# Optimization experiments

Measured on AMD Instinct MI355X. Metric: run time of the kernel, lower is better.

## Reference

```python
import jax, jax.numpy as jnp
import numpy as np
from jax import lax
from jax.scipy.linalg import expm

B, T, H, NCLS = 256, 784, 512, 10


def setup_inputs() -> dict:
    key = jax.random.key(0)
    ks = jax.random.split(key, 6)
    inputs = jax.random.normal(ks[0], (B, T), dtype=jnp.float32)
    # faithful to Model: fixed permutation from RandomState(92916)
    permutation = jnp.asarray(np.random.RandomState(92916).permutation(T), dtype=jnp.int64)
    W_skew = jax.random.normal(ks[1], (H, H), dtype=jnp.float32) * 0.05  # free param for skew-symmetric A
    W_in = jax.random.normal(ks[2], (H, 1), dtype=jnp.float32)            # Linear(1, H, bias=False)
    b_mod = jax.random.uniform(ks[3], (H,), dtype=jnp.float32, minval=-0.01, maxval=0.01)  # modrelu bias
    W_lin = jax.random.normal(ks[4], (NCLS, H), dtype=jnp.float32) * 0.05
    b_lin = jax.random.normal(ks[5], (NCLS,), dtype=jnp.float32) * 0.05
    return {"inputs": inputs, "permutation": permutation, "W_skew": W_skew,
            "W_in": W_in, "b_mod": b_mod, "W_lin": W_lin, "b_lin": b_lin}


def reference(inputs, permutation, W_skew, W_in, b_mod, W_lin, b_lin):
    # permuted-pixel input sequence: [B, T]
    x = inputs[:, permutation]
    # expm parametrization of the orthogonal recurrent kernel:
    # A = triu(W,1) - triu(W,1)^T (skew-symmetric), Borth = expm(A) is orthogonal
    Au = jnp.triu(W_skew, 1)
    Borth = expm(Au - Au.T)  # [H, H]
    # precompute all input projections: Linear(1,H) on each scalar pixel -> [T, B, H]
    proj = x.T[:, :, None] * W_in[:, 0][None, None, :]

    def step(h, u):
        pre = u + h @ Borth                                  # [B, H]
        h_new = jnp.sign(pre) * jax.nn.relu(jnp.abs(pre) + b_mod)  # modrelu
        return h_new, None

    h0 = jnp.zeros((inputs.shape[0], W_in.shape[0]), dtype=inputs.dtype)
    hT, _ = lax.scan(step, h0, proj)
    return hT @ W_lin.T + b_lin  # [B, 10]
```

## Files before the change

kernel.cpp:

```cpp
#include <hip/hip_runtime.h>

#define TSTEPS 784
#define BATCH  256
#define HDIM   512
#define NCLS   10
#define NGRP   16
#define WGPG   8

typedef __bf16 bf16x8 __attribute__((ext_vector_type(8)));
typedef float  f32x4  __attribute__((ext_vector_type(4)));
typedef unsigned uint4v __attribute__((ext_vector_type(4)));
typedef unsigned long long u64;
typedef unsigned short u16;

static __device__ __forceinline__ u16 f2bf(float f) {
  unsigned u = __builtin_bit_cast(unsigned, f);
  u += 0x7fffu + ((u >> 16) & 1u);
  return (u16)(u >> 16);
}
static __device__ __forceinline__ float bf2f(unsigned s) {
  unsigned u = s << 16;
  return __builtin_bit_cast(float, u);
}

__global__ __launch_bounds__(256) void gather_xp(const float* __restrict__ in,
                                                 const int* __restrict__ perm,
                                                 float* __restrict__ xp) {
  int t = blockIdx.x;
  int b = threadIdx.x;
  int p = perm[t];
  p = (p < 0) ? 0 : (p >= TSTEPS ? TSTEPS - 1 : p);
  xp[t * BATCH + b] = in[b * TSTEPS + p];
}

__global__ __launch_bounds__(256) void build_X(const float* __restrict__ W,
                                               float* __restrict__ X) {
  int idx = blockIdx.x * 256 + threadIdx.x;
  int i = idx >> 9, j = idx & 511;
  float v = 0.f;
  if (j > i) v = W[i * HDIM + j];
  else if (i > j) v = -W[j * HDIM + i];
  X[idx] = v * 0.03125f;
}

__global__ __launch_bounds__(256) void axpyI(float* __restrict__ P,
                                             const float* __restrict__ X, float coef) {
  int idx = blockIdx.x * 256 + threadIdx.x;
  int i = idx >> 9, j = idx & 511;
  P[idx] = coef * X[idx] + ((i == j) ? 1.f : 0.f);
}

__global__ __launch_bounds__(256) void gemm512(float* __restrict__ C,
                                               const float* __restrict__ A,
                                               const float* __restrict__ B,
                                               float alpha, int addI) {
  __shared__ float As[16][68];
  __shared__ float Bs[16][68];
  const int tx = threadIdx.x, ty = threadIdx.y;
  const int tid = ty * 16 + tx;
  const int ib = blockIdx.y, jb = blockIdx.x;
  const int ra = tid >> 2, ca = (tid & 3) << 2;
  const int rb = tid >> 4, cb = (tid & 15) << 2;
  float acc[4][4] = {};
  for (int kt = 0; kt < HDIM / 16; ++kt) {
    f32x4 av = *(const f32x4*)(A + (ib * 64 + ra) * HDIM + kt * 16 + ca);
    f32x4 bv = *(const f32x4*)(B + (kt * 16 + rb) * HDIM + jb * 64 + cb);
    __syncthreads();
    As[ca + 0][ra] = av[0];
    As[ca + 1][ra] = av[1];
    As[ca + 2][ra] = av[2];
    As[ca + 3][ra] = av[3];
    *(f32x4*)&Bs[rb][cb] = bv;
    __syncthreads();
#pragma unroll
    for (int kk = 0; kk < 16; ++kk) {
      f32x4 a4 = *(const f32x4*)&As[kk][ty << 2];
      f32x4 b4 = *(const f32x4*)&Bs[kk][tx << 2];
#pragma unroll
      for (int u = 0; u < 4; ++u)
#pragma unroll
        for (int v = 0; v < 4; ++v) acc[u][v] = fmaf(a4[u], b4[v], acc[u][v]);
    }
  }
#pragma unroll
  for (int u = 0; u < 4; ++u)
#pragma unroll
    for (int v = 0; v < 4; ++v) {
      int r = ib * 64 + (ty << 2) + u, c = jb * 64 + (tx << 2) + v;
      float val = alpha * acc[u][v];
      if (addI && r == c) val += 1.f;
      C[r * HDIM + c] = val;
    }
}

__global__ __launch_bounds__(256, 1) void rnn_main(
    const float* __restrict__ xp, const float* __restrict__ Borth,
    const float* __restrict__ W_in, const float* __restrict__ b_mod,
    const float* __restrict__ W_lin, const float* __restrict__ b_lin,
    u16* __restrict__ h0hi, u16* __restrict__ h0lo, u16* __restrict__ h1hi,
    u16* __restrict__ h1lo, unsigned* __restrict__ flags, float* __restrict__ out) {
  __shared__ unsigned tileHi[4096], tileLo[4096];

  const int wg = blockIdx.x;
  const int gb = wg & 15;
  const int cg = wg >> 4;
  const int tid = threadIdx.x;
  const int wave = tid >> 6;
  const int lane = tid & 63;
  const int quad = lane >> 4;
  const int l16 = lane & 15;
  const int colg = (cg << 6) + (wave << 4) + l16;

  bf16x8 Bfh[16], Bfl[16];
#pragma unroll
  for (int ki = 0; ki < 16; ++ki) {
#pragma unroll
    for (int j = 0; j < 8; ++j) {
      int k = (ki << 5) + (quad << 3) + j;
      float v = Borth[k * HDIM + colg];
      u16 hb = f2bf(v);
      u16 lb = f2bf(v - bf2f(hb));
      Bfh[ki][j] = __builtin_bit_cast(__bf16, hb);
      Bfl[ki][j] = __builtin_bit_cast(__bf16, lb);
    }
  }
  const float win = W_in[colg];
  const float bm = b_mod[colg];

  u16* const g0h = h0hi + (gb << 13);
  u16* const g0l = h0lo + (gb << 13);
  u16* const g1h = h1hi + (gb << 13);
  u16* const g1l = h1lo + (gb << 13);
  unsigned* const myflag = flags + ((gb << 3) + cg) * 32;
  unsigned* const gflags = flags + (gb << 3) * 32;
  const unsigned swz = (unsigned)((l16 & 7) << 2);

  for (int t = 0; t < TSTEPS; ++t) {
    const u64* __restrict__ cH = (const u64*)((t & 1) ? g1h : g0h);
    const u64* __restrict__ cL = (const u64*)((t & 1) ? g1l : g0l);
    u16* __restrict__ nH = (t & 1) ? g0h : g1h;
    u16* __restrict__ nL = (t & 1) ? g0l : g1l;

    u64 qh[8], ql[8];
#pragma unroll
    for (int i = 0; i < 8; ++i) {
      qh[i] = __hip_atomic_load(cH + tid + (i << 8), __ATOMIC_RELAXED,
                                __HIP_MEMORY_SCOPE_AGENT);
      ql[i] = __hip_atomic_load(cL + tid + (i << 8), __ATOMIC_RELAXED,
                                __HIP_MEMORY_SCOPE_AGENT);
    }
#pragma unroll
    for (int i = 0; i < 8; ++i) {
      int f = tid + (i << 8);
      int r = f >> 7;
      unsigned du = (unsigned)(f & 127) << 1;
      unsigned phys = ((unsigned)r << 8) | (du ^ ((r & 7) << 2));
      *(u64*)(tileHi + phys) = qh[i];
      *(u64*)(tileLo + phys) = ql[i];
    }
    __syncthreads();

    f32x4 a_hh = {0.f, 0.f, 0.f, 0.f};
    f32x4 a_lh = {0.f, 0.f, 0.f, 0.f};
    f32x4 a_hl = {0.f, 0.f, 0.f, 0.f};
#pragma unroll
    for (int ki = 0; ki < 16; ++ki) {
      unsigned dcol0 = (unsigned)((ki << 4) + (quad << 2));
      unsigned off = ((unsigned)l16 << 8) + (dcol0 ^ swz);
      bf16x8 ah = __builtin_bit_cast(bf16x8, *(const uint4v*)(tileHi + off));
      bf16x8 al = __builtin_bit_cast(bf16x8, *(const uint4v*)(tileLo + off));
      a_hh = __builtin_amdgcn_mfma_f32_16x16x32_bf16(ah, Bfh[ki], a_hh, 0, 0, 0);
      a_lh = __builtin_amdgcn_mfma_f32_16x16x32_bf16(al, Bfh[ki], a_lh, 0, 0, 0);
      a_hl = __builtin_amdgcn_mfma_f32_16x16x32_bf16(ah, Bfl[ki], a_hl, 0, 0, 0);
    }

    const f32x4 xps = *(const f32x4*)(xp + t * BATCH + (gb << 4) + (quad << 2));
#pragma unroll
    for (int r = 0; r < 4; ++r) {
      float pre = a_hh[r] + a_lh[r] + a_hl[r] + xps[r] * win;
      float mm = fmaxf(fabsf(pre) + bm, 0.f);
      float hv = (pre > 0.f) ? mm : ((pre < 0.f) ? -mm : 0.f);
      int idx = (((quad << 2) + r) << 9) + colg;
      u16 hbv = f2bf(hv);
      u16 lbv = f2bf(hv - bf2f(hbv));
      __hip_atomic_store(nH + idx, hbv, __ATOMIC_RELAXED, __HIP_MEMORY_SCOPE_AGENT);
      __hip_atomic_store(nL + idx, lbv, __ATOMIC_RELAXED, __HIP_MEMORY_SCOPE_AGENT);
    }

    asm volatile("s_waitcnt vmcnt(0)" ::: "memory");
    __syncthreads();
    if (tid == 0)
      __hip_atomic_store(myflag, (unsigned)(t + 1), __ATOMIC_RELAXED,
                         __HIP_MEMORY_SCOPE_AGENT);
    const unsigned target = (unsigned)(t + 1);
    int spin = 0;
    for (;;) {
      unsigned fl = __hip_atomic_load(gflags + (lane & 7) * 32, __ATOMIC_RELAXED,
                                      __HIP_MEMORY_SCOPE_AGENT);
      if (__ballot(fl >= target) == ~0ull) break;
      __builtin_amdgcn_s_sleep(1);
      if (++spin > (1 << 22)) break;
    }
  }

  if (cg == 0) {
    int row = tid >> 4;
    int cls = tid & 15;
    if (cls < NCLS) {
      const u16* hh = g0h + (row << 9);
      const u16* hl = g0l + (row << 9);
      float s = b_lin[cls];
      const float* wl = W_lin + cls * HDIM;
      for (int k = 0; k < HDIM; ++k) {
        unsigned hu = __hip_atomic_load(hh + k, __ATOMIC_RELAXED, __HIP_MEMORY_SCOPE_AGENT);
        unsigned lu = __hip_atomic_load(hl + k, __ATOMIC_RELAXED, __HIP_MEMORY_SCOPE_AGENT);
        s = fmaf(bf2f(hu) + bf2f(lu), wl[k], s);
      }
      out[((gb << 4) + row) * NCLS + cls] = s;
    }
  }
}

extern "C" void kernel_launch(void* const* d_in, const int* in_sizes, int n_in,
                              void* d_out, int out_size, void* d_ws, size_t ws_size,
                              hipStream_t stream) {
  const float* inputs = (const float*)d_in[0];
  const int* perm = (const int*)d_in[1];
  const float* W_skew = (const float*)d_in[2];
  const float* W_in = (const float*)d_in[3];
  const float* b_mod = (const float*)d_in[4];
  const float* W_lin = (const float*)d_in[5];
  const float* b_lin = (const float*)d_in[6];
  float* out = (float*)d_out;

  char* ws = (char*)d_ws;
  unsigned* flags = (unsigned*)ws;
  u16* h0hi = (u16*)(ws + 32768);
  u16* h0lo = h0hi + BATCH * HDIM;
  u16* h1hi = h0lo + BATCH * HDIM;
  u16* h1lo = h1hi + BATCH * HDIM;
  float* xp = (float*)(h1lo + BATCH * HDIM);
  float* X = xp + TSTEPS * BATCH;
  float* P = X + HDIM * HDIM;
  float* Q = P + HDIM * HDIM;

  hipMemsetAsync(flags, 0, 32768, stream);
  hipMemsetAsync(h0hi, 0, (size_t)BATCH * HDIM * 2 * sizeof(u16), stream);

  gather_xp<<<TSTEPS, 256, 0, stream>>>(inputs, perm, xp);
  build_X<<<(HDIM * HDIM) / 256, 256, 0, stream>>>(W_skew, X);

  axpyI<<<(HDIM * HDIM) / 256, 256, 0, stream>>>(P, X, 1.f / 6.f);
  float* a = P;
  float* b = Q;
  for (int k = 5; k >= 1; --k) {
    gemm512<<<dim3(8, 8), dim3(16, 16), 0, stream>>>(b, X, a, 1.f / (float)k, 1);
    float* tmp = a; a = b; b = tmp;
  }
  for (int i = 0; i < 5; ++i) {
    gemm512<<<dim3(8, 8), dim3(16, 16), 0, stream>>>(b, a, a, 1.f, 0);
    float* tmp = a; a = b; b = tmp;
  }

  rnn_main<<<NGRP * WGPG, 256, 0, stream>>>(xp, a, W_in, b_mod, W_lin, b_lin,
                                            h0hi, h0lo, h1hi, h1lo, flags, out);
  (void)in_sizes; (void)n_in; (void)out_size; (void)ws_size;
}
```

Baseline: 2.595 ms.

## Process two batch groups per workgroup to overlap recurrence of independent groups

Halves the grid so each workgroup handles two independent 16-row batch groups (A and B) in sequence within every timestep. Group A's flag is published before group B's compute starts, so other workgroups can proceed on A while B runs, and both groups' loads are issued together up front. The MFMA operand order is swapped so each lane owns four consecutive hidden columns, which allows packed 64-bit stores instead of scalar 16-bit stores. It also shortens the spin timeout and reads the final hidden state through LDS. The cost is twice the per-workgroup serial work on half as many CUs, plus more LDS and registers.

After: 4.453 ms. +71.6%, slower.

```diff
diff --git a/kernel.cpp b/kernel.cpp
--- a/kernel.cpp
+++ b/kernel.cpp
@@ -6,6 +6,7 @@
 #define NCLS   10
 #define NGRP   16
 #define WGPG   8
+#define NPAIR  8
 
 typedef __bf16 bf16x8 __attribute__((ext_vector_type(8)));
 typedef float  f32x4  __attribute__((ext_vector_type(4)));
@@ -99,17 +100,20 @@
     const float* __restrict__ W_lin, const float* __restrict__ b_lin,
     u16* __restrict__ h0hi, u16* __restrict__ h0lo, u16* __restrict__ h1hi,
     u16* __restrict__ h1lo, unsigned* __restrict__ flags, float* __restrict__ out) {
-  __shared__ unsigned tileHi[4096], tileLo[4096];
+  __shared__ unsigned tHiA[4096], tLoA[4096];
+  __shared__ unsigned tHiB[4096], tLoB[4096];
 
   const int wg = blockIdx.x;
-  const int gb = wg & 15;
-  const int cg = wg >> 4;
+  const int pr = wg & (NPAIR - 1);
+  const int cg = wg >> 3;
+  const int gbA = pr << 1, gbB = (pr << 1) | 1;
   const int tid = threadIdx.x;
   const int wave = tid >> 6;
   const int lane = tid & 63;
   const int quad = lane >> 4;
   const int l16 = lane & 15;
   const int colg = (cg << 6) + (wave << 4) + l16;
+  const int hbase = (cg << 6) + (wave << 4) + (quad << 2);
 
   bf16x8 Bfh[16], Bfl[16];
 #pragma unroll
@@ -124,99 +128,198 @@
       Bfl[ki][j] = __builtin_bit_cast(__bf16, lb);
     }
   }
-  const float win = W_in[colg];
-  const float bm = b_mod[colg];
-
-  u16* const g0h = h0hi + (gb << 13);
-  u16* const g0l = h0lo + (gb << 13);
-  u16* const g1h = h1hi + (gb << 13);
-  u16* const g1l = h1lo + (gb << 13);
-  unsigned* const myflag = flags + ((gb << 3) + cg) * 32;
-  unsigned* const gflags = flags + (gb << 3) * 32;
+  const f32x4 win4 = *(const f32x4*)(W_in + hbase);
+  const f32x4 bm4 = *(const f32x4*)(b_mod + hbase);
+
+  u16* const g0hA = h0hi + (gbA << 13);
+  u16* const g0lA = h0lo + (gbA << 13);
+  u16* const g1hA = h1hi + (gbA << 13);
+  u16* const g1lA = h1lo + (gbA << 13);
+  u16* const g0hB = h0hi + (gbB << 13);
+  u16* const g0lB = h0lo + (gbB << 13);
+  u16* const g1hB = h1hi + (gbB << 13);
+  u16* const g1lB = h1lo + (gbB << 13);
+  unsigned* const myflagA = flags + (((gbA << 3) + cg) << 5);
+  unsigned* const myflagB = flags + (((gbB << 3) + cg) << 5);
+  unsigned* const poll = flags + ((gbA << 3) << 5);
   const unsigned swz = (unsigned)((l16 & 7) << 2);
 
   for (int t = 0; t < TSTEPS; ++t) {
-    const u64* __restrict__ cH = (const u64*)((t & 1) ? g1h : g0h);
-    const u64* __restrict__ cL = (const u64*)((t & 1) ? g1l : g0l);
-    u16* __restrict__ nH = (t & 1) ? g0h : g1h;
-    u16* __restrict__ nL = (t & 1) ? g0l : g1l;
-
-    u64 qh[8], ql[8];
+    const u64* __restrict__ cHA = (const u64*)((t & 1) ? g1hA : g0hA);
+    const u64* __restrict__ cLA = (const u64*)((t & 1) ? g1lA : g0lA);
+    u16* __restrict__ nHA = (t & 1) ? g0hA : g1hA;
+    u16* __restrict__ nLA = (t & 1) ? g0lA : g1lA;
+    const u64* __restrict__ cHB = (const u64*)((t & 1) ? g1hB : g0hB);
+    const u64* __restrict__ cLB = (const u64*)((t & 1) ? g1lB : g0lB);
+    u16* __restrict__ nHB = (t & 1) ? g0hB : g1hB;
+    u16* __restrict__ nLB = (t & 1) ? g0lB : g1lB;
+
+    u64 qhA[8], qlA[8], qhB[8], qlB[8];
 #pragma unroll
     for (int i = 0; i < 8; ++i) {
-      qh[i] = __hip_atomic_load(cH + tid + (i << 8), __ATOMIC_RELAXED,
-                                __HIP_MEMORY_SCOPE_AGENT);
-      ql[i] = __hip_atomic_load(cL + tid + (i << 8), __ATOMIC_RELAXED,
-                                __HIP_MEMORY_SCOPE_AGENT);
-    }
+      qhA[i] = __hip_atomic_load(cHA + tid + (i << 8), __ATOMIC_RELAXED,
+                                 __HIP_MEMORY_SCOPE_AGENT);
+      qlA[i] = __hip_atomic_load(cLA + tid + (i << 8), __ATOMIC_RELAXED,
+                                 __HIP_MEMORY_SCOPE_AGENT);
+    }
+#pragma unroll
+    for (int i = 0; i < 8; ++i) {
+      qhB[i] = __hip_atomic_load(cHB + tid + (i << 8), __ATOMIC_RELAXED,
+                                 __HIP_MEMORY_SCOPE_AGENT);
+      qlB[i] = __hip_atomic_load(cLB + tid + (i << 8), __ATOMIC_RELAXED,
+                                 __HIP_MEMORY_SCOPE_AGENT);
+    }
+
 #pragma unroll
     for (int i = 0; i < 8; ++i) {
       int f = tid + (i << 8);
       int r = f >> 7;
       unsigned du = (unsigned)(f & 127) << 1;
       unsigned phys = ((unsigned)r << 8) | (du ^ ((r & 7) << 2));
-      *(u64*)(tileHi + phys) = qh[i];
-      *(u64*)(tileLo + phys) = ql[i];
-    }
-    __syncthreads();
-
-    f32x4 a_hh = {0.f, 0.f, 0.f, 0.f};
-    f32x4 a_lh = {0.f, 0.f, 0.f, 0.f};
-    f32x4 a_hl = {0.f, 0.f, 0.f, 0.f};
+      *(u64*)(tHiA + phys) = qhA[i];
+      *(u64*)(tLoA + phys) = qlA[i];
+    }
+    __syncthreads();
+
+    f32x4 hhA = {0.f, 0.f, 0.f, 0.f};
+    f32x4 lhA = {0.f, 0.f, 0.f, 0.f};
+    f32x4 hlA = {0.f, 0.f, 0.f, 0.f};
 #pragma unroll
     for (int ki = 0; ki < 16; ++ki) {
       unsigned dcol0 = (unsigned)((ki << 4) + (quad << 2));
       unsigned off = ((unsigned)l16 << 8) + (dcol0 ^ swz);
-      bf16x8 ah = __builtin_bit_cast(bf16x8, *(const uint4v*)(tileHi + off));
-      bf16x8 al = __builtin_bit_cast(bf16x8, *(const uint4v*)(tileLo + off));
-      a_hh = __builtin_amdgcn_mfma_f32_16x16x32_bf16(ah, Bfh[ki], a_hh, 0, 0, 0);
-      a_lh = __builtin_amdgcn_mfma_f32_16x16x32_bf16(al, Bfh[ki], a_lh, 0, 0, 0);
-      a_hl = __builtin_amdgcn_mfma_f32_16x16x32_bf16(ah, Bfl[ki], a_hl, 0, 0, 0);
-    }
-
-    const f32x4 xps = *(const f32x4*)(xp + t * BATCH + (gb << 4) + (quad << 2));
-#pragma unroll
-    for (int r = 0; r < 4; ++r) {
-      float pre = a_hh[r] + a_lh[r] + a_hl[r] + xps[r] * win;
-      float mm = fmaxf(fabsf(pre) + bm, 0.f);
-      float hv = (pre > 0.f) ? mm : ((pre < 0.f) ? -mm : 0.f);
-      int idx = (((quad << 2) + r) << 9) + colg;
-      u16 hbv = f2bf(hv);
-      u16 lbv = f2bf(hv - bf2f(hbv));
-      __hip_atomic_store(nH + idx, hbv, __ATOMIC_RELAXED, __HIP_MEMORY_SCOPE_AGENT);
-      __hip_atomic_store(nL + idx, lbv, __ATOMIC_RELAXED, __HIP_MEMORY_SCOPE_AGENT);
-    }
-
+      bf16x8 ah = __builtin_bit_cast(bf16x8, *(const uint4v*)(tHiA + off));
+      bf16x8 al = __builtin_bit_cast(bf16x8, *(const uint4v*)(tLoA + off));
+      hhA = __builtin_amdgcn_mfma_f32_16x16x32_bf16(Bfh[ki], ah, hhA, 0, 0, 0);
+      lhA = __builtin_amdgcn_mfma_f32_16x16x32_bf16(Bfh[ki], al, lhA, 0, 0, 0);
+      hlA = __builtin_amdgcn_mfma_f32_16x16x32_bf16(Bfl[ki], ah, hlA, 0, 0, 0);
+    }
+    {
+      float xs = xp[t * BATCH + (gbA << 4) + l16];
+      u64 hw = 0, lw = 0;
+#pragma unroll
+      for (int r = 0; r < 4; ++r) {
+        float pre = hhA[r] + lhA[r] + hlA[r] + xs * win4[r];
+        float mm = fmaxf(fabsf(pre) + bm4[r], 0.f);
+        float hv = (pre > 0.f) ? mm : ((pre < 0.f) ? -mm : 0.f);
+        u16 hbv = f2bf(hv);
+        u16 lbv = f2bf(hv - bf2f(hbv));
+        hw |= ((u64)hbv) << (16 * r);
+        lw |= ((u64)lbv) << (16 * r);
+      }
+      int idx = (l16 << 9) + hbase;
+      __hip_atomic_store((u64*)(nHA + idx), hw, __ATOMIC_RELAXED,
+                         __HIP_MEMORY_SCOPE_AGENT);
+      __hip_atomic_store((u64*)(nLA + idx), lw, __ATOMIC_RELAXED,
+                         __HIP_MEMORY_SCOPE_AGENT);
+    }
     asm volatile("s_waitcnt vmcnt(0)" ::: "memory");
     __syncthreads();
     if (tid == 0)
-      __hip_atomic_store(myflag, (unsigned)(t + 1), __ATOMIC_RELAXED,
-                         __HIP_MEMORY_SCOPE_AGENT);
+      __hip_atomic_store(myflagA, (unsigned)(t + 1), __ATOMIC_RELAXED,
+                         __HIP_MEMORY_SCOPE_AGENT);
+
+#pragma unroll
+    for (int i = 0; i < 8; ++i) {
+      int f = tid + (i << 8);
+      int r = f >> 7;
+      unsigned du = (unsigned)(f & 127) << 1;
+      unsigned phys = ((unsigned)r << 8) | (du ^ ((r & 7) << 2));
+      *(u64*)(tHiB + phys) = qhB[i];
+      *(u64*)(tLoB + phys) = qlB[i];
+    }
+    __syncthreads();
+
+    f32x4 hhB = {0.f, 0.f, 0.f, 0.f};
+    f32x4 lhB = {0.f, 0.f, 0.f, 0.f};
+    f32x4 hlB = {0.f, 0.f, 0.f, 0.f};
+#pragma unroll
+    for (int ki = 0; ki < 16; ++ki) {
+      unsigned dcol0 = (unsigned)((ki << 4) + (quad << 2));
+      unsigned off = ((unsigned)l16 << 8) + (dcol0 ^ swz);
+      bf16x8 ah = __builtin_bit_cast(bf16x8, *(const uint4v*)(tHiB + off));
+      bf16x8 al = __builtin_bit_cast(bf16x8, *(const uint4v*)(tLoB + off));
+      hhB = __builtin_amdgcn_mfma_f32_16x16x32_bf16(Bfh[ki], ah, hhB, 0, 0, 0);
+      lhB = __builtin_amdgcn_mfma_f32_16x16x32_bf16(Bfh[ki], al, lhB, 0, 0, 0);
+      hlB = __builtin_amdgcn_mfma_f32_16x16x32_bf16(Bfl[ki], ah, hlB, 0, 0, 0);
+    }
+    {
+      float xs = xp[t * BATCH + (gbB << 4) + l16];
+      u64 hw = 0, lw = 0;
+#pragma unroll
+      for (int r = 0; r < 4; ++r) {
+        float pre = hhB[r] + lhB[r] + hlB[r] + xs * win4[r];
+        float mm = fmaxf(fabsf(pre) + bm4[r], 0.f);
+        float hv = (pre > 0.f) ? mm : ((pre < 0.f) ? -mm : 0.f);
+        u16 hbv = f2bf(hv);
+        u16 lbv = f2bf(hv - bf2f(hbv));
+        hw |= ((u64)hbv) << (16 * r);
+        lw |= ((u64)lbv) << (16 * r);
+      }
+      int idx = (l16 << 9) + hbase;
+      __hip_atomic_store((u64*)(nHB + idx), hw, __ATOMIC_RELAXED,
+                         __HIP_MEMORY_SCOPE_AGENT);
+      __hip_atomic_store((u64*)(nLB + idx), lw, __ATOMIC_RELAXED,
+                         __HIP_MEMORY_SCOPE_AGENT);
+    }
+    asm volatile("s_waitcnt vmcnt(0)" ::: "memory");
+    __syncthreads();
+    if (tid == 0)
+      __hip_atomic_store(myflagB, (unsigned)(t + 1), __ATOMIC_RELAXED,
+                         __HIP_MEMORY_SCOPE_AGENT);
+
     const unsigned target = (unsigned)(t + 1);
     int spin = 0;
     for (;;) {
-      unsigned fl = __hip_atomic_load(gflags + (lane & 7) * 32, __ATOMIC_RELAXED,
+      unsigned fl = __hip_atomic_load(poll + ((lane & 15) << 5), __ATOMIC_RELAXED,
                                       __HIP_MEMORY_SCOPE_AGENT);
       if (__ballot(fl >= target) == ~0ull) break;
       __builtin_amdgcn_s_sleep(1);
-      if (++spin > (1 << 22)) break;
-    }
+      if (++spin > (1 << 15)) break;
+    }
+    __builtin_amdgcn_sched_barrier(0);
   }
 
   if (cg == 0) {
-    int row = tid >> 4;
-    int cls = tid & 15;
-    if (cls < NCLS) {
-      const u16* hh = g0h + (row << 9);
-      const u16* hl = g0l + (row << 9);
-      float s = b_lin[cls];
-      const float* wl = W_lin + cls * HDIM;
-      for (int k = 0; k < HDIM; ++k) {
-        unsigned hu = __hip_atomic_load(hh + k, __ATOMIC_RELAXED, __HIP_MEMORY_SCOPE_AGENT);
-        unsigned lu = __hip_atomic_load(hl + k, __ATOMIC_RELAXED, __HIP_MEMORY_SCOPE_AGENT);
-        s = fmaf(bf2f(hu) + bf2f(lu), wl[k], s);
-      }
-      out[((gb << 4) + row) * NCLS + cls] = s;
+#pragma unroll 1
+    for (int sel = 0; sel < 2; ++sel) {
+      const u64* fH = (const u64*)(sel ? g0hB : g0hA);
+      const u64* fL = (const u64*)(sel ? g0lB : g0lA);
+      const int gb = sel ? gbB : gbA;
+      __syncthreads();
+      u64 qh[8], ql[8];
+#pragma unroll
+      for (int i = 0; i < 8; ++i) {
+        qh[i] = __hip_atomic_load(fH + tid + (i << 8), __ATOMIC_RELAXED,
+                                  __HIP_MEMORY_SCOPE_AGENT);
+        ql[i] = __hip_atomic_load(fL + tid + (i << 8), __ATOMIC_RELAXED,
+                                  __HIP_MEMORY_SCOPE_AGENT);
+      }
+#pragma unroll
+      for (int i = 0; i < 8; ++i) {
+        int f = tid + (i << 8);
+        int r = f >> 7;
+        unsigned du = (unsigned)(f & 127) << 1;
+        unsigned phys = ((unsigned)r << 8) | (du ^ ((r & 7) << 2));
+        *(u64*)(tHiA + phys) = qh[i];
+        *(u64*)(tLoA + phys) = ql[i];
+      }
+      __syncthreads();
+      int row = tid >> 4;
+      int cls = tid & 15;
+      if (cls < NCLS) {
+        float acc = b_lin[cls];
+        const float* wl = W_lin + cls * HDIM;
+        for (int k = 0; k < HDIM; ++k) {
+          unsigned phys = ((unsigned)row << 8) |
+                          (((unsigned)k >> 1) ^ (((unsigned)row & 7) << 2));
+          unsigned sh = ((unsigned)k & 1) << 4;
+          float hv = bf2f((tHiA[phys] >> sh) & 0xFFFFu) +
+                     bf2f((tLoA[phys] >> sh) & 0xFFFFu);
+          acc = fmaf(hv, wl[k], acc);
+        }
+        out[((gb << 4) + row) * NCLS + cls] = acc;
+      }
     }
   }
 }
@@ -262,7 +365,7 @@
     float* tmp = a; a = b; b = tmp;
   }
 
-  rnn_main<<<NGRP * WGPG, 256, 0, stream>>>(xp, a, W_in, b_mod, W_lin, b_lin,
-                                            h0hi, h0lo, h1hi, h1lo, flags, out);
+  rnn_main<<<NPAIR * WGPG, 256, 0, stream>>>(xp, a, W_in, b_mod, W_lin, b_lin,
+                                             h0hi, h0lo, h1hi, h1lo, flags, out);
   (void)in_sizes; (void)n_in; (void)out_size; (void)ws_size;
 }
```

## Replace per-step flag barrier with tagged data polling and packed hi/lo state

Applied to the files above, without the earlier changes.

Drops the per-step flag store, vmcnt wait, __syncthreads and flag-spin barrier. Instead each consumer spins on the hidden-state buffer itself, where the LSB of each packed word carries a parity tag marking which step wrote it. The hi/lo bf16 halves are packed into one 32-bit word, so each step needs a single dwordx4 store and fewer loads, and LDS tiles are double-buffered. The aim is to take synchronisation latency off the serial recurrence. The cost is one bit of low-part precision, the assumption that 16-byte stores become visible atomically, and a much shorter spin timeout that could exit early under contention.

New measurement: 2.994 ms. 15.4% more time.

```diff
diff --git a/kernel.cpp b/kernel.cpp
--- a/kernel.cpp
+++ b/kernel.cpp
@@ -97,9 +97,9 @@
     const float* __restrict__ xp, const float* __restrict__ Borth,
     const float* __restrict__ W_in, const float* __restrict__ b_mod,
     const float* __restrict__ W_lin, const float* __restrict__ b_lin,
-    u16* __restrict__ h0hi, u16* __restrict__ h0lo, u16* __restrict__ h1hi,
-    u16* __restrict__ h1lo, unsigned* __restrict__ flags, float* __restrict__ out) {
-  __shared__ unsigned tileHi[4096], tileLo[4096];
+    unsigned* __restrict__ h0, unsigned* __restrict__ h1,
+    float* __restrict__ out) {
+  __shared__ unsigned tile0[8192], tile1[8192];
 
   const int wg = blockIdx.x;
   const int gb = wg & 15;
@@ -110,6 +110,7 @@
   const int quad = lane >> 4;
   const int l16 = lane & 15;
   const int colg = (cg << 6) + (wave << 4) + l16;
+  const int hbase = (cg << 6) + (wave << 4) + (quad << 2);
 
   bf16x8 Bfh[16], Bfl[16];
 #pragma unroll
@@ -124,99 +125,170 @@
       Bfl[ki][j] = __builtin_bit_cast(__bf16, lb);
     }
   }
-  const float win = W_in[colg];
-  const float bm = b_mod[colg];
-
-  u16* const g0h = h0hi + (gb << 13);
-  u16* const g0l = h0lo + (gb << 13);
-  u16* const g1h = h1hi + (gb << 13);
-  u16* const g1l = h1lo + (gb << 13);
-  unsigned* const myflag = flags + ((gb << 3) + cg) * 32;
-  unsigned* const gflags = flags + (gb << 3) * 32;
+  const f32x4 win4 = *(const f32x4*)(W_in + hbase);
+  const f32x4 bm4 = *(const f32x4*)(b_mod + hbase);
+
+  const u64 b0 = (u64)(h0 + (gb << 13));
+  const u64 b1 = (u64)(h1 + (gb << 13));
+  const unsigned vo0 = (unsigned)((tid + 0 * 256) << 4);
+  const unsigned vo1 = (unsigned)((tid + 1 * 256) << 4);
+  const unsigned vo2 = (unsigned)((tid + 2 * 256) << 4);
+  const unsigned vo3 = (unsigned)((tid + 3 * 256) << 4);
+  const unsigned vo4 = (unsigned)((tid + 4 * 256) << 4);
+  const unsigned vo5 = (unsigned)((tid + 5 * 256) << 4);
+  const unsigned vo6 = (unsigned)((tid + 6 * 256) << 4);
+  const unsigned vo7 = (unsigned)((tid + 7 * 256) << 4);
+  const unsigned soff = (unsigned)(((l16 << 9) + hbase) << 2);
   const unsigned swz = (unsigned)((l16 & 7) << 2);
 
   for (int t = 0; t < TSTEPS; ++t) {
-    const u64* __restrict__ cH = (const u64*)((t & 1) ? g1h : g0h);
-    const u64* __restrict__ cL = (const u64*)((t & 1) ? g1l : g0l);
-    u16* __restrict__ nH = (t & 1) ? g0h : g1h;
-    u16* __restrict__ nL = (t & 1) ? g0l : g1l;
-
-    u64 qh[8], ql[8];
-#pragma unroll
-    for (int i = 0; i < 8; ++i) {
-      qh[i] = __hip_atomic_load(cH + tid + (i << 8), __ATOMIC_RELAXED,
-                                __HIP_MEMORY_SCOPE_AGENT);
-      ql[i] = __hip_atomic_load(cL + tid + (i << 8), __ATOMIC_RELAXED,
-                                __HIP_MEMORY_SCOPE_AGENT);
-    }
-#pragma unroll
-    for (int i = 0; i < 8; ++i) {
-      int f = tid + (i << 8);
-      int r = f >> 7;
-      unsigned du = (unsigned)(f & 127) << 1;
-      unsigned phys = ((unsigned)r << 8) | (du ^ ((r & 7) << 2));
-      *(u64*)(tileHi + phys) = qh[i];
-      *(u64*)(tileLo + phys) = ql[i];
-    }
-    __syncthreads();
-
-    f32x4 a_hh = {0.f, 0.f, 0.f, 0.f};
-    f32x4 a_lh = {0.f, 0.f, 0.f, 0.f};
-    f32x4 a_hl = {0.f, 0.f, 0.f, 0.f};
-#pragma unroll
-    for (int ki = 0; ki < 16; ++ki) {
-      unsigned dcol0 = (unsigned)((ki << 4) + (quad << 2));
-      unsigned off = ((unsigned)l16 << 8) + (dcol0 ^ swz);
-      bf16x8 ah = __builtin_bit_cast(bf16x8, *(const uint4v*)(tileHi + off));
-      bf16x8 al = __builtin_bit_cast(bf16x8, *(const uint4v*)(tileLo + off));
-      a_hh = __builtin_amdgcn_mfma_f32_16x16x32_bf16(ah, Bfh[ki], a_hh, 0, 0, 0);
-      a_lh = __builtin_amdgcn_mfma_f32_16x16x32_bf16(al, Bfh[ki], a_lh, 0, 0, 0);
-      a_hl = __builtin_amdgcn_mfma_f32_16x16x32_bf16(ah, Bfl[ki], a_hl, 0, 0, 0);
-    }
-
-    const f32x4 xps = *(const f32x4*)(xp + t * BATCH + (gb << 4) + (quad << 2));
-#pragma unroll
-    for (int r = 0; r < 4; ++r) {
-      float pre = a_hh[r] + a_lh[r] + a_hl[r] + xps[r] * win;
-      float mm = fmaxf(fabsf(pre) + bm, 0.f);
-      float hv = (pre > 0.f) ? mm : ((pre < 0.f) ? -mm : 0.f);
-      int idx = (((quad << 2) + r) << 9) + colg;
-      u16 hbv = f2bf(hv);
-      u16 lbv = f2bf(hv - bf2f(hbv));
-      __hip_atomic_store(nH + idx, hbv, __ATOMIC_RELAXED, __HIP_MEMORY_SCOPE_AGENT);
-      __hip_atomic_store(nL + idx, lbv, __ATOMIC_RELAXED, __HIP_MEMORY_SCOPE_AGENT);
-    }
-
-    asm volatile("s_waitcnt vmcnt(0)" ::: "memory");
-    __syncthreads();
-    if (tid == 0)
-      __hip_atomic_store(myflag, (unsigned)(t + 1), __ATOMIC_RELAXED,
-                         __HIP_MEMORY_SCOPE_AGENT);
-    const unsigned target = (unsigned)(t + 1);
+    const u64 rb = (t & 1) ? b1 : b0;
+    const u64 wb = (t & 1) ? b0 : b1;
+    const unsigned rtag = (unsigned)((t >> 1) & 1);
+    const unsigned wtag = (unsigned)(((t + 1) >> 1) & 1);
+    unsigned* const tl = (t & 1) ? tile1 : tile0;
+
+    uint4v q0, q1, q2, q3, q4, q5, q6, q7;
     int spin = 0;
     for (;;) {
-      unsigned fl = __hip_atomic_load(gflags + (lane & 7) * 32, __ATOMIC_RELAXED,
-                                      __HIP_MEMORY_SCOPE_AGENT);
-      if (__ballot(fl >= target) == ~0ull) break;
+      asm volatile(
+          "global_load_dwordx4 %[q0], %[v0], %[b] sc1\n\t"
+          "global_load_dwordx4 %[q1], %[v1], %[b] sc1\n\t"
+          "global_load_dwordx4 %[q2], %[v2], %[b] sc1\n\t"
+          "global_load_dwordx4 %[q3], %[v3], %[b] sc1\n\t"
+          "global_load_dwordx4 %[q4], %[v4], %[b] sc1\n\t"
+          "global_load_dwordx4 %[q5], %[v5], %[b] sc1\n\t"
+          "global_load_dwordx4 %[q6], %[v6], %[b] sc1\n\t"
+          "global_load_dwordx4 %[q7], %[v7], %[b] sc1\n\t"
+          "s_waitcnt vmcnt(0)"
+          : [q0] "=&v"(q0), [q1] "=&v"(q1), [q2] "=&v"(q2), [q3] "=&v"(q3),
+            [q4] "=&v"(q4), [q5] "=&v"(q5), [q6] "=&v"(q6), [q7] "=&v"(q7)
+          : [v0] "v"(vo0), [v1] "v"(vo1), [v2] "v"(vo2), [v3] "v"(vo3),
+            [v4] "v"(vo4), [v5] "v"(vo5), [v6] "v"(vo6), [v7] "v"(vo7),
+            [b] "s"(rb));
+      unsigned bad = 0;
+#define TCHK(q) bad |= (q[0] ^ rtag) | (q[1] ^ rtag) | (q[2] ^ rtag) | (q[3] ^ rtag)
+      TCHK(q0); TCHK(q1); TCHK(q2); TCHK(q3);
+      TCHK(q4); TCHK(q5); TCHK(q6); TCHK(q7);
+#undef TCHK
+      if (!(bad & 1u)) break;
       __builtin_amdgcn_s_sleep(1);
-      if (++spin > (1 << 22)) break;
+      if (++spin > (1 << 11)) break;
+    }
+    __builtin_amdgcn_sched_barrier(0);
+
+#define STG(g, q)                                                      \
+  {                                                                    \
+    int G = tid + ((g) << 8);                                          \
+    int r = G >> 7;                                                    \
+    unsigned dc = (unsigned)(G & 127) << 2;                            \
+    unsigned phys = ((unsigned)r << 9) | (dc ^ ((unsigned)(r & 7) << 2)); \
+    *(uint4v*)(tl + phys) = q;                                         \
+  }
+    STG(0, q0) STG(1, q1) STG(2, q2) STG(3, q3)
+    STG(4, q4) STG(5, q5) STG(6, q6) STG(7, q7)
+#undef STG
+    __syncthreads();
+
+    f32x4 hh = {0.f, 0.f, 0.f, 0.f};
+    f32x4 lh = {0.f, 0.f, 0.f, 0.f};
+    f32x4 hl = {0.f, 0.f, 0.f, 0.f};
+#pragma unroll
+    for (int ki = 0; ki < 16; ++ki) {
+      unsigned dc0 = (unsigned)((ki << 5) + (quad << 3));
+      unsigned base = (unsigned)l16 << 9;
+      unsigned offL = base + (dc0 ^ swz);
+      unsigned offH = base + ((dc0 + 4) ^ swz);
+      uint4v e0 = *(const uint4v*)(tl + offL);
+      uint4v e1 = *(const uint4v*)(tl + offH);
+      uint4v ahv, alv;
+      ahv[0] = __builtin_amdgcn_perm(e0[1], e0[0], 0x07060302u);
+      ahv[1] = __builtin_amdgcn_perm(e0[3], e0[2], 0x07060302u);
+      ahv[2] = __builtin_amdgcn_perm(e1[1], e1[0], 0x07060302u);
+      ahv[3] = __builtin_amdgcn_perm(e1[3], e1[2], 0x07060302u);
+      alv[0] = __builtin_amdgcn_perm(e0[1], e0[0], 0x05040100u);
+      alv[1] = __builtin_amdgcn_perm(e0[3], e0[2], 0x05040100u);
+      alv[2] = __builtin_amdgcn_perm(e1[1], e1[0], 0x05040100u);
+      alv[3] = __builtin_amdgcn_perm(e1[3], e1[2], 0x05040100u);
+      bf16x8 ah = __builtin_bit_cast(bf16x8, ahv);
+      bf16x8 al = __builtin_bit_cast(bf16x8, alv);
+      hh = __builtin_amdgcn_mfma_f32_16x16x32_bf16(Bfh[ki], ah, hh, 0, 0, 0);
+      lh = __builtin_amdgcn_mfma_f32_16x16x32_bf16(Bfh[ki], al, lh, 0, 0, 0);
+      hl = __builtin_amdgcn_mfma_f32_16x16x32_bf16(Bfl[ki], ah, hl, 0, 0, 0);
+    }
+
+    {
+      float xs = xp[t * BATCH + (gb << 4) + l16];
+      uint4v sv;
+#pragma unroll
+      for (int r = 0; r < 4; ++r) {
+        float pre = hh[r] + lh[r] + hl[r] + xs * win4[r];
+        float mm = fmaxf(fabsf(pre) + bm4[r], 0.f);
+        float hv = (pre > 0.f) ? mm : ((pre < 0.f) ? -mm : 0.f);
+        u16 hbv = f2bf(hv);
+        u16 lbv = f2bf(hv - bf2f(hbv));
+        sv[r] = ((unsigned)hbv << 16) | (unsigned)((lbv & 0xFFFEu) | wtag);
+      }
+      asm volatile("global_store_dwordx4 %[o], %[d], %[b] sc1" ::[o] "v"(soff),
+                   [d] "v"(sv), [b] "s"(wb));
     }
   }
 
   if (cg == 0) {
+    uint4v q0, q1, q2, q3, q4, q5, q6, q7;
+    const unsigned rtag = 0u;
+    int spin = 0;
+    for (;;) {
+      asm volatile(
+          "global_load_dwordx4 %[q0], %[v0], %[b] sc1\n\t"
+          "global_load_dwordx4 %[q1], %[v1], %[b] sc1\n\t"
+          "global_load_dwordx4 %[q2], %[v2], %[b] sc1\n\t"
+          "global_load_dwordx4 %[q3], %[v3], %[b] sc1\n\t"
+          "global_load_dwordx4 %[q4], %[v4], %[b] sc1\n\t"
+          "global_load_dwordx4 %[q5], %[v5], %[b] sc1\n\t"
+          "global_load_dwordx4 %[q6], %[v6], %[b] sc1\n\t"
+          "global_load_dwordx4 %[q7], %[v7], %[b] sc1\n\t"
+          "s_waitcnt vmcnt(0)"
+          : [q0] "=&v"(q0), [q1] "=&v"(q1), [q2] "=&v"(q2), [q3] "=&v"(q3),
+            [q4] "=&v"(q4), [q5] "=&v"(q5), [q6] "=&v"(q6), [q7] "=&v"(q7)
+          : [v0] "v"(vo0), [v1] "v"(vo1), [v2] "v"(vo2), [v3] "v"(vo3),
+            [v4] "v"(vo4), [v5] "v"(vo5), [v6] "v"(vo6), [v7] "v"(vo7),
+            [b] "s"(b0));
+      unsigned bad = 0;
+#define TCHK(q) bad |= (q[0] ^ rtag) | (q[1] ^ rtag) | (q[2] ^ rtag) | (q[3] ^ rtag)
+      TCHK(q0); TCHK(q1); TCHK(q2); TCHK(q3);
+      TCHK(q4); TCHK(q5); TCHK(q6); TCHK(q7);
+#undef TCHK
+      if (!(bad & 1u)) break;
+      __builtin_amdgcn_s_sleep(1);
+      if (++spin > (1 << 11)) break;
+    }
+    __builtin_amdgcn_sched_barrier(0);
+#define STG(g, q)                                                      \
+  {                                                                    \
+    int G = tid + ((g) << 8);                                          \
+    int r = G >> 7;                                                    \
+    unsigned dc = (unsigned)(G & 127) << 2;                            \
+    unsigned phys = ((unsigned)r << 9) | (dc ^ ((unsigned)(r & 7) << 2)); \
+    *(uint4v*)(tile0 + phys) = q;                                      \
+  }
+    STG(0, q0) STG(1, q1) STG(2, q2) STG(3, q3)
+    STG(4, q4) STG(5, q5) STG(6, q6) STG(7, q7)
+#undef STG
+    __syncthreads();
     int row = tid >> 4;
     int cls = tid & 15;
     if (cls < NCLS) {
-      const u16* hh = g0h + (row << 9);
-      const u16* hl = g0l + (row << 9);
-      float s = b_lin[cls];
+      float acc = b_lin[cls];
       const float* wl = W_lin + cls * HDIM;
       for (int k = 0; k < HDIM; ++k) {
-        unsigned hu = __hip_atomic_load(hh + k, __ATOMIC_RELAXED, __HIP_MEMORY_SCOPE_AGENT);
-        unsigned lu = __hip_atomic_load(hl + k, __ATOMIC_RELAXED, __HIP_MEMORY_SCOPE_AGENT);
-        s = fmaf(bf2f(hu) + bf2f(lu), wl[k], s);
+        unsigned phys = ((unsigned)row << 9) |
+                        ((unsigned)k ^ (((unsigned)row & 7) << 2));
+        unsigned x = tile0[phys];
+        float hv = bf2f(x >> 16) + bf2f(x & 0xFFFFu);
+        acc = fmaf(hv, wl[k], acc);
       }
-      out[((gb << 4) + row) * NCLS + cls] = s;
+      out[((gb << 4) + row) * NCLS + cls] = acc;
     }
   }
 }
@@ -234,18 +306,15 @@
   float* out = (float*)d_out;
 
   char* ws = (char*)d_ws;
-  unsigned* flags = (unsigned*)ws;
-  u16* h0hi = (u16*)(ws + 32768);
-  u16* h0lo = h0hi + BATCH * HDIM;
-  u16* h1hi = h0lo + BATCH * HDIM;
-  u16* h1lo = h1hi + BATCH * HDIM;
-  float* xp = (float*)(h1lo + BATCH * HDIM);
+  unsigned* h0 = (unsigned*)ws;
+  unsigned* h1 = h0 + BATCH * HDIM;
+  float* xp = (float*)(h1 + BATCH * HDIM);
   float* X = xp + TSTEPS * BATCH;
   float* P = X + HDIM * HDIM;
   float* Q = P + HDIM * HDIM;
 
-  hipMemsetAsync(flags, 0, 32768, stream);
-  hipMemsetAsync(h0hi, 0, (size_t)BATCH * HDIM * 2 * sizeof(u16), stream);
+  hipMemsetAsync(h0, 0, (size_t)BATCH * HDIM * 4, stream);
+  hipMemsetAsync(h1, 0x01, (size_t)BATCH * HDIM * 4, stream);
 
   gather_xp<<<TSTEPS, 256, 0, stream>>>(inputs, perm, xp);
   build_X<<<(HDIM * HDIM) / 256, 256, 0, stream>>>(W_skew, X);
@@ -263,6 +332,6 @@
   }
 
   rnn_main<<<NGRP * WGPG, 256, 0, stream>>>(xp, a, W_in, b_mod, W_lin, b_lin,
-                                            h0hi, h0lo, h1hi, h1lo, flags, out);
+                                            h0, h1, out);
   (void)in_sizes; (void)n_in; (void)out_size; (void)ws_size;
 }
```
